# Kernel tuning notes

Measured on AMD Instinct MI355X. Metric: run time of the kernel, lower is better.

Reference implementation:

```python
import jax, jax.numpy as jnp
import numpy as np

OPACITY_FACTOR = 0.8  # module-level global `opacity_factor` in the original repo


def setup_inputs() -> dict:
    key = jax.random.key(0)
    N, H, W = 128, 512, 512
    # Pre-rendered RGBA polygons (stand-in for Polygon(...)(h, w, param2img)),
    # values in [0,1]; channel 3 is alpha.
    polys = jax.random.uniform(key, (N, 1, 4, H, W), dtype=jnp.float32)
    return {"polys": polys, "h": H, "w": W}


def reference(polys, h, w):
    # canvas = ones((1,4,h,w)); sequentially alpha-composite each polygon:
    # canvas = canvas*(1 - alpha*op) + alpha*op*poly, alpha = poly[:,3:]
    canvas0 = jnp.ones((1, 4, h, w), dtype=polys.dtype)

    def step(canvas, poly):  # poly: (1,4,h,w)
        a = poly[:, 3:] * OPACITY_FACTOR  # (1,1,h,w), broadcasts over RGBA
        return canvas * (1.0 - a) + a * poly, None

    canvas, _ = jax.lax.scan(step, canvas0, polys)
    return canvas
```

## Files before the change

kernel.cpp:

```cpp
#include <hip/hip_runtime.h>


#define PH 512
#define PW 512
#define PHW (PH * PW)
#define PHW4 (PHW / 4)
#define OPACITY 0.8f

__device__ __forceinline__ void composite(float4& c, const float4& p, const float4& a) {
    c.x = fmaf(a.x, p.x - c.x, c.x);
    c.y = fmaf(a.y, p.y - c.y, c.y);
    c.z = fmaf(a.z, p.z - c.z, c.z);
    c.w = fmaf(a.w, p.w - c.w, c.w);
}

__global__ __launch_bounds__(256) void paint_kernel(const float4* __restrict__ polys,
                                                    float4* __restrict__ out,
                                                    int n_polys) {
    const int idx = blockIdx.x * blockDim.x + threadIdx.x;
    if (idx >= PHW4) return;

    const float4 one = make_float4(1.f, 1.f, 1.f, 1.f);
    float4 c0 = one, c1 = one, c2 = one, c3 = one;

    const float4* p = polys + idx;
    #pragma unroll 4
    for (int n = 0; n < n_polys; ++n) {
        const float4 p0 = p[0 * PHW4];
        const float4 p1 = p[1 * PHW4];
        const float4 p2 = p[2 * PHW4];
        const float4 p3 = p[3 * PHW4];
        p += 4 * PHW4;

        const float4 a = make_float4(p3.x * OPACITY, p3.y * OPACITY,
                                     p3.z * OPACITY, p3.w * OPACITY);
        composite(c0, p0, a);
        composite(c1, p1, a);
        composite(c2, p2, a);
        composite(c3, p3, a);
    }

    out[0 * PHW4 + idx] = c0;
    out[1 * PHW4 + idx] = c1;
    out[2 * PHW4 + idx] = c2;
    out[3 * PHW4 + idx] = c3;
}

extern "C" void kernel_launch(void* const* d_in, const int* in_sizes, int n_in,
                              void* d_out, int out_size, void* d_ws, size_t ws_size,
                              hipStream_t stream) {
    const float* polys = (const float*)d_in[0];
    float* out = (float*)d_out;

    const int n_polys = in_sizes[0] / (4 * PHW);

    const int threads = 256;
    const int blocks = (PHW4 + threads - 1) / threads;
    paint_kernel<<<blocks, threads, 0, stream>>>((const float4*)polys,
                                                 (float4*)out, n_polys);
}
```

Before: 667.0 us.

## Split polygon sequence across waves using associative affine composite scan

```diff
diff --git a/kernel.cpp b/kernel.cpp
--- a/kernel.cpp
+++ b/kernel.cpp
@@ -6,56 +6,78 @@
 #define PHW (PH * PW)
 #define PHW4 (PHW / 4)
 #define OPACITY 0.8f
+#define NWAVES 4
 
-__device__ __forceinline__ void composite(float4& c, const float4& p, const float4& a) {
-    c.x = fmaf(a.x, p.x - c.x, c.x);
-    c.y = fmaf(a.y, p.y - c.y, c.y);
-    c.z = fmaf(a.z, p.z - c.z, c.z);
-    c.w = fmaf(a.w, p.w - c.w, c.w);
-}
+__device__ __forceinline__ float4 f4(float v) { return make_float4(v, v, v, v); }
 
-__global__ __launch_bounds__(256) void paint_kernel(const float4* __restrict__ polys,
-                                                    float4* __restrict__ out,
-                                                    int n_polys) {
-    const int idx = blockIdx.x * blockDim.x + threadIdx.x;
-    if (idx >= PHW4) return;
+__global__ __launch_bounds__(256, 4) void paint_kernel(const float4* __restrict__ polys,
+                                                       float4* __restrict__ out,
+                                                       int n_polys) {
+    __shared__ float4 sA[NWAVES][64];
+    __shared__ float4 sB[NWAVES][4][64];
+    const int lane = threadIdx.x & 63;
+    const int wave = threadIdx.x >> 6;
+    const int gidx = blockIdx.x * 64 + lane;
 
-    const float4 one = make_float4(1.f, 1.f, 1.f, 1.f);
-    float4 c0 = one, c1 = one, c2 = one, c3 = one;
+    const int L = n_polys / NWAVES;
+    const int lstart = wave * L;
+    const int lend = (wave == NWAVES - 1) ? n_polys : lstart + L;
 
-    const float4* p = polys + idx;
+    float4 A = f4(1.f);
+    float4 B0 = f4(0.f), B1 = f4(0.f), B2 = f4(0.f), B3 = f4(0.f);
+
+    const float4* p = polys + (size_t)lstart * 4 * PHW4 + gidx;
     #pragma unroll 4
-    for (int n = 0; n < n_polys; ++n) {
+    for (int n = lstart; n < lend; ++n) {
         const float4 p0 = p[0 * PHW4];
         const float4 p1 = p[1 * PHW4];
         const float4 p2 = p[2 * PHW4];
         const float4 p3 = p[3 * PHW4];
         p += 4 * PHW4;
 
-        const float4 a = make_float4(p3.x * OPACITY, p3.y * OPACITY,
-                                     p3.z * OPACITY, p3.w * OPACITY);
-        composite(c0, p0, a);
-        composite(c1, p1, a);
-        composite(c2, p2, a);
-        composite(c3, p3, a);
+        const float4 a  = make_float4(p3.x * OPACITY, p3.y * OPACITY,
+                                      p3.z * OPACITY, p3.w * OPACITY);
+        const float4 om = make_float4(1.f - a.x, 1.f - a.y, 1.f - a.z, 1.f - a.w);
+
+        A.x *= om.x; A.y *= om.y; A.z *= om.z; A.w *= om.w;
+        B0.x = fmaf(a.x, p0.x, om.x * B0.x); B0.y = fmaf(a.y, p0.y, om.y * B0.y);
+        B0.z = fmaf(a.z, p0.z, om.z * B0.z); B0.w = fmaf(a.w, p0.w, om.w * B0.w);
+        B1.x = fmaf(a.x, p1.x, om.x * B1.x); B1.y = fmaf(a.y, p1.y, om.y * B1.y);
+        B1.z = fmaf(a.z, p1.z, om.z * B1.z); B1.w = fmaf(a.w, p1.w, om.w * B1.w);
+        B2.x = fmaf(a.x, p2.x, om.x * B2.x); B2.y = fmaf(a.y, p2.y, om.y * B2.y);
+        B2.z = fmaf(a.z, p2.z, om.z * B2.z); B2.w = fmaf(a.w, p2.w, om.w * B2.w);
+        B3.x = fmaf(a.x, p3.x, om.x * B3.x); B3.y = fmaf(a.y, p3.y, om.y * B3.y);
+        B3.z = fmaf(a.z, p3.z, om.z * B3.z); B3.w = fmaf(a.w, p3.w, om.w * B3.w);
     }
 
-    out[0 * PHW4 + idx] = c0;
-    out[1 * PHW4 + idx] = c1;
-    out[2 * PHW4 + idx] = c2;
-    out[3 * PHW4 + idx] = c3;
+    sA[wave][lane] = A;
+    sB[wave][0][lane] = B0;
+    sB[wave][1][lane] = B1;
+    sB[wave][2][lane] = B2;
+    sB[wave][3][lane] = B3;
+    __syncthreads();
+
+    const int ch = wave;
+    float4 c = f4(1.f);
+    #pragma unroll
+    for (int w = 0; w < NWAVES; ++w) {
+        const float4 a4 = sA[w][lane];
+        const float4 b4 = sB[w][ch][lane];
+        c.x = fmaf(a4.x, c.x, b4.x);
+        c.y = fmaf(a4.y, c.y, b4.y);
+        c.z = fmaf(a4.z, c.z, b4.z);
+        c.w = fmaf(a4.w, c.w, b4.w);
+    }
+    out[(size_t)ch * PHW4 + gidx] = c;
 }
 
 extern "C" void kernel_launch(void* const* d_in, const int* in_sizes, int n_in,
                               void* d_out, int out_size, void* d_ws, size_t ws_size,
                               hipStream_t stream) {
-    const float* polys = (const float*)d_in[0];
-    float* out = (float*)d_out;
-
+    const float4* polys = (const float4*)d_in[0];
+    float4* out = (float4*)d_out;
     const int n_polys = in_sizes[0] / (4 * PHW);
 
-    const int threads = 256;
-    const int blocks = (PHW4 + threads - 1) / threads;
-    paint_kernel<<<blocks, threads, 0, stream>>>((const float4*)polys,
-                                                 (float4*)out, n_polys);
+    const int blocks = PHW4 / 64;
+    paint_kernel<<<blocks, 256, 0, stream>>>(polys, out, n_polys);
 }
```

Result: no change. 673.0 us (+0.9%).
